# Kernel tuning notes

Measured on AMD Instinct MI355X. Metric: run time of the kernel, lower is better.

The kernel has to match this reference:

```python
import jax, jax.numpy as jnp
import numpy as np

D_MODEL = 1024
NUM_HEADS = 16
D_K = D_MODEL // NUM_HEADS
THETA = 10000.0


def _apply_rope(x, positions):
    # x: [B, H, S, d_k], positions: [B, S]
    dk = x.shape[-1]
    freq = 1.0 / (THETA ** (jnp.arange(0, dk, 2, dtype=jnp.float32) / dk))  # [dk/2]
    ang = positions.astype(jnp.float32)[:, None, :, None] * freq  # [B,1,S,dk/2]
    cos, sin = jnp.cos(ang), jnp.sin(ang)
    x_even = x[..., 0::2]
    x_odd = x[..., 1::2]
    re = x_even * cos - x_odd * sin
    ro = x_even * sin + x_odd * cos
    # interleave back: [..., dk/2, 2] -> [..., dk]
    return jnp.stack([re, ro], axis=-1).reshape(x.shape)


def setup_inputs() -> dict:
    key = jax.random.key(0)
    kx, kq, kk, kv, ko = jax.random.split(key, 5)
    B, S = 2, 2048
    std = (2.0 / (D_MODEL + D_MODEL)) ** 0.5
    x = jax.random.normal(kx, (B, S, D_MODEL), dtype=jnp.float32)
    Wq = jax.random.normal(kq, (D_MODEL, D_MODEL), dtype=jnp.float32) * std
    Wk = jax.random.normal(kk, (D_MODEL, D_MODEL), dtype=jnp.float32) * std
    Wv = jax.random.normal(kv, (D_MODEL, D_MODEL), dtype=jnp.float32) * std
    Wo = jax.random.normal(ko, (D_MODEL, D_MODEL), dtype=jnp.float32) * std
    token_positions = jnp.tile(jnp.arange(S, dtype=jnp.int32)[None, :], (B, 1))
    return {"x": x, "Wq": Wq, "Wk": Wk, "Wv": Wv, "Wo": Wo,
            "token_positions": token_positions}


def reference(x, Wq, Wk, Wv, Wo, token_positions):
    B, S, D = x.shape
    H, dk = NUM_HEADS, D_K
    scale = 1.0 / np.sqrt(dk)
    # Linear is y = x @ W.T with W:[d_out, d_in]
    q = jnp.einsum('bsd,ed->bse', x, Wq).reshape(B, S, H, dk).transpose(0, 2, 1, 3)
    k = jnp.einsum('bsd,ed->bse', x, Wk).reshape(B, S, H, dk).transpose(0, 2, 1, 3)
    v = jnp.einsum('bsd,ed->bse', x, Wv).reshape(B, S, H, dk).transpose(0, 2, 1, 3)
    q = _apply_rope(q, token_positions)
    k = _apply_rope(k, token_positions)
    scores = jnp.einsum('bhqd,bhkd->bhqk', q, k) * scale  # [B,H,S,S]
    causal = jnp.tril(jnp.ones((S, S), dtype=bool))
    scores = jnp.where(causal[None, None, :, :], scores, -jnp.inf)
    probs = jax.nn.softmax(scores, axis=-1)
    attn = jnp.einsum('bhqk,bhkd->bhqd', probs, v)  # [B,H,S,dk]
    attn = attn.transpose(0, 2, 1, 3).reshape(B, S, D)
    return jnp.einsum('bsd,ed->bse', attn, Wo)
```

## Files before the change

### kernel.cpp

```cpp
#include <hip/hip_runtime.h>
#include <hip/hip_bf16.h>
#include <math.h>

#define B_  2
#define S_  2048
#define H_  16
#define D_  1024
#define DK_ 64

typedef __attribute__((ext_vector_type(8))) short bf16x8;
typedef __attribute__((ext_vector_type(8))) unsigned short ushort8v;
typedef __attribute__((ext_vector_type(4))) float f32x4;

__device__ __forceinline__ unsigned short f2bf(float f) {
  unsigned u = __float_as_uint(f);
  unsigned r = (u + 0x7FFFu + ((u >> 16) & 1u)) >> 16;
  return (unsigned short)r;
}
__device__ __forceinline__ unsigned pack_trunc(float lo, float hi) {
  return (__float_as_uint(lo) >> 16) | (__float_as_uint(hi) & 0xffff0000u);
}
__device__ __forceinline__ float fast_exp2(float x) {
#if __has_builtin(__builtin_amdgcn_exp2f)
  return __builtin_amdgcn_exp2f(x);
#else
  return __expf(x * 0.69314718056f);
#endif
}
__device__ __forceinline__ void gload_lds16(const unsigned short* g,
                                            unsigned short* l) {
  __builtin_amdgcn_global_load_lds(
      (const __attribute__((address_space(1))) unsigned int*)(const void*)g,
      (__attribute__((address_space(3))) unsigned int*)(void*)l, 16, 0, 0);
}

__global__ __launch_bounds__(256)
void cast5_bf16(const float* __restrict__ x,  const float* __restrict__ wq,
                const float* __restrict__ wk, const float* __restrict__ wv,
                const float* __restrict__ wo,
                unsigned short* __restrict__ xb,  unsigned short* __restrict__ wqb,
                unsigned short* __restrict__ wkb, unsigned short* __restrict__ wvb,
                unsigned short* __restrict__ wob)
{
  const int idx = blockIdx.x;
  const float* s; unsigned short* d; int lblk;
  if (idx < 2048) { s = x; d = xb; lblk = idx; }
  else {
    int t = idx - 2048;
    int w = t >> 9;
    lblk  = t & 511;
    s = (w == 0) ? wq  : (w == 1) ? wk  : (w == 2) ? wv  : wo;
    d = (w == 0) ? wqb : (w == 1) ? wkb : (w == 2) ? wvb : wob;
  }
  size_t i0 = ((size_t)lblk * 256 + threadIdx.x) * 8;
  float4 v0 = *(const float4*)(s + i0);
  float4 v1 = *(const float4*)(s + i0 + 4);
  ushort8v o;
  o[0] = f2bf(v0.x); o[1] = f2bf(v0.y); o[2] = f2bf(v0.z); o[3] = f2bf(v0.w);
  o[4] = f2bf(v1.x); o[5] = f2bf(v1.y); o[6] = f2bf(v1.z); o[7] = f2bf(v1.w);
  *(ushort8v*)(d + i0) = o;
}

__global__ __launch_bounds__(256)
void gemm_qkv(const unsigned short* __restrict__ A0,
              const unsigned short* __restrict__ W0,
              const unsigned short* __restrict__ W1,
              const unsigned short* __restrict__ W2,
              unsigned short* __restrict__ qh,
              unsigned short* __restrict__ kh,
              unsigned short* __restrict__ vt,
              const int* __restrict__ tp)
{
  const int z    = blockIdx.z;
  const int flat = blockIdx.y * 8 + blockIdx.x;
  const int xcd  = flat & 7;
  const int u    = flat >> 3;

  int row0, col0;
  if (z < 2) {
    row0 = (xcd * 8 + (u & 7)) * 64;
    col0 = (u >> 3) * 128;
  } else {
    int tc = xcd * 4 + (u & 3);
    int cr = u >> 2;
    row0 = cr * 64;
    col0 = tc * 128;
  }
  const unsigned short* Aptr = (z == 2) ? W2 : A0;
  const unsigned short* Bptr = (z == 0) ? W0 : (z == 1) ? W1 : A0;

  __shared__ unsigned short As[64 * 64];
  __shared__ unsigned short Bs[128 * 64];
  __shared__ int tps[64];

  const int tid   = threadIdx.x;
  const int wave  = tid >> 6;
  const int lane  = tid & 63;
  const int quad  = lane >> 4;
  const int col16 = lane & 15;
  const int wr    = (wave >> 1) * 32;
  const int wc    = (wave & 1) * 64;

  if (z < 2 && tid < 64) tps[tid] = tp[row0 + tid];

  const int srow = wave * 8 + (lane >> 3);
  const int scol = ((lane & 7) ^ ((lane >> 3) & 7)) * 8;
  const unsigned short* gA = Aptr + (size_t)(row0 + srow) * D_ + scol;
  const unsigned short* gB = Bptr + (size_t)(col0 + srow) * D_ + scol;

  f32x4 acc[2][4];
  #pragma unroll
  for (int mt = 0; mt < 2; ++mt)
    #pragma unroll
    for (int nt = 0; nt < 4; ++nt)
      #pragma unroll
      for (int r = 0; r < 4; ++r) acc[mt][nt][r] = 0.f;

  for (int k0 = 0; k0 < D_; k0 += 64) {
    __syncthreads();
    #pragma unroll
    for (int p = 0; p < 2; ++p)
      gload_lds16(gA + (size_t)(p * 32) * D_ + k0, &As[(p * 32 + wave * 8) * 64]);
    #pragma unroll
    for (int p = 0; p < 4; ++p)
      gload_lds16(gB + (size_t)(p * 32) * D_ + k0, &Bs[(p * 32 + wave * 8) * 64]);
    __syncthreads();

    #pragma unroll
    for (int h = 0; h < 2; ++h) {
      const int jo = ((h * 4 + quad) ^ (col16 & 7)) * 8;
      bf16x8 af[2], bfr[4];
      #pragma unroll
      for (int mt = 0; mt < 2; ++mt)
        af[mt] = *(const bf16x8*)&As[(wr + mt * 16 + col16) * 64 + jo];
      #pragma unroll
      for (int nt = 0; nt < 4; ++nt)
        bfr[nt] = *(const bf16x8*)&Bs[(wc + nt * 16 + col16) * 64 + jo];

      #pragma unroll
      for (int mt = 0; mt < 2; ++mt)
        #pragma unroll
        for (int nt = 0; nt < 4; ++nt)
          acc[mt][nt] = __builtin_amdgcn_mfma_f32_16x16x32_bf16(
              af[mt], bfr[nt], acc[mt][nt], 0, 0, 0);
    }
  }

  if (z == 2) {
    #pragma unroll
    for (int mt = 0; mt < 2; ++mt)
      #pragma unroll
      for (int r = 0; r < 4; ++r) {
        int c = row0 + wr + mt * 16 + quad * 4 + r;
        int h = c >> 6, d = c & 63;
        #pragma unroll
        for (int nt = 0; nt < 4; ++nt) {
          int t  = col0 + wc + nt * 16 + col16;
          int bb = t >> 11, sl = t & (S_ - 1);
          vt[((size_t)((bb << 4) + h) * DK_ + d) * S_ + sl] =
              f2bf(acc[mt][nt][r]);
        }
      }
  } else {
    unsigned short* C = z ? kh : qh;
    const float qs = z ? 1.0f : 0.1803368801111204f;
    const float sgn = (col16 & 1) ? 1.f : -1.f;
    float freqr[4];
    #pragma unroll
    for (int nt = 0; nt < 4; ++nt) {
      int i = ((wc + nt * 16 + col16) & 63) >> 1;
      freqr[nt] = exp2f(-0.4152410118f * (float)i);
    }
    #pragma unroll
    for (int mt = 0; mt < 2; ++mt)
      #pragma unroll
      for (int r = 0; r < 4; ++r) {
        int rl  = wr + mt * 16 + quad * 4 + r;
        int row = row0 + rl;
        float p = (float)tps[rl];
        #pragma unroll
        for (int nt = 0; nt < 4; ++nt) {
          int col = col0 + wc + nt * 16 + col16;
          float ang = p * freqr[nt];
          float sn = __sinf(ang), cs = __cosf(ang);
          float val = acc[mt][nt][r];
          float oth = __shfl_xor(val, 1);
          C[(size_t)row * D_ + col] = f2bf((val * cs + oth * sgn * sn) * qs);
        }
      }
  }
}

__global__ __launch_bounds__(256, 8)
void gemm_wo(const unsigned short* __restrict__ A,
             const unsigned short* __restrict__ W,
             float* __restrict__ C)
{
  __shared__ unsigned short As[64 * 64];
  __shared__ unsigned short Bs[64 * 64];

  const int flat = blockIdx.y * 16 + blockIdx.x;
  const int xcd  = flat & 7;
  const int u    = flat >> 3;
  const int by   = xcd * 8 + (u & 7);
  const int bx   = u >> 3;

  const int tid   = threadIdx.x;
  const int wave  = tid >> 6;
  const int lane  = tid & 63;
  const int quad  = lane >> 4;
  const int col16 = lane & 15;
  const int row0  = by * 64;
  const int col0  = bx * 64;
  const int wr    = (wave >> 1) * 32;
  const int wc    = (wave & 1) * 32;

  const int srow = wave * 8 + (lane >> 3);
  const int scol = ((lane & 7) ^ ((lane >> 3) & 7)) * 8;
  const unsigned short* gA = A + (size_t)(row0 + srow) * D_ + scol;
  const unsigned short* gB = W + (size_t)(col0 + srow) * D_ + scol;

  f32x4 acc[2][2];
  #pragma unroll
  for (int mt = 0; mt < 2; ++mt)
    #pragma unroll
    for (int nt = 0; nt < 2; ++nt)
      #pragma unroll
      for (int r = 0; r < 4; ++r) acc[mt][nt][r] = 0.f;

  for (int k0 = 0; k0 < D_; k0 += 64) {
    __syncthreads();
    #pragma unroll
    for (int p = 0; p < 2; ++p) {
      gload_lds16(gA + (size_t)(p * 32) * D_ + k0, &As[(p * 32 + wave * 8) * 64]);
      gload_lds16(gB + (size_t)(p * 32) * D_ + k0, &Bs[(p * 32 + wave * 8) * 64]);
    }
    __syncthreads();

    #pragma unroll
    for (int h = 0; h < 2; ++h) {
      const int jo = ((h * 4 + quad) ^ (col16 & 7)) * 8;
      bf16x8 af[2], bfr[2];
      #pragma unroll
      for (int mt = 0; mt < 2; ++mt)
        af[mt] = *(const bf16x8*)&As[(wr + mt * 16 + col16) * 64 + jo];
      #pragma unroll
      for (int nt = 0; nt < 2; ++nt)
        bfr[nt] = *(const bf16x8*)&Bs[(wc + nt * 16 + col16) * 64 + jo];

      #pragma unroll
      for (int mt = 0; mt < 2; ++mt)
        #pragma unroll
        for (int nt = 0; nt < 2; ++nt)
          acc[mt][nt] = __builtin_amdgcn_mfma_f32_16x16x32_bf16(
              af[mt], bfr[nt], acc[mt][nt], 0, 0, 0);
    }
  }

  #pragma unroll
  for (int mt = 0; mt < 2; ++mt)
    #pragma unroll
    for (int r = 0; r < 4; ++r) {
      int row = row0 + wr + mt * 16 + quad * 4 + r;
      #pragma unroll
      for (int nt = 0; nt < 2; ++nt) {
        int col = col0 + wc + nt * 16 + col16;
        C[(size_t)row * D_ + col] = acc[mt][nt][r];
      }
    }
}

__global__ __launch_bounds__(512, 8)
void attn_mfma(const unsigned short* __restrict__ Q,
               const unsigned short* __restrict__ K,
               const unsigned short* __restrict__ Vt,
               unsigned short* __restrict__ O)
{
  const int f   = blockIdx.x;
  const int qt  = 31 - (f >> 5);
  const int bh  = f & 31;
  const int b   = bh >> 4, h = bh & 15;

  const int tid  = threadIdx.x;
  const int w    = tid >> 6;
  const int lane = tid & 63;
  const int quad = lane >> 4;
  const int col  = lane & 15;
  const int rw   = w & 3;
  const int p    = w >> 2;
  const int qlocal = rw * 16 + col;

  __shared__ unsigned short Ks[2 * 4096];
  __shared__ unsigned short Vs[2 * 4096];
  __shared__ __align__(16) unsigned short Pl[8][16][72];

  const size_t qkbase = (size_t)b * S_ * D_ + (size_t)h * DK_;
  const size_t vtbase = (size_t)bh * DK_ * S_;

  const int qrow = qt * 64 + qlocal;
  bf16x8 qf[2];
  qf[0] = *(const bf16x8*)(Q + qkbase + (size_t)qrow * D_ + quad * 8);
  qf[1] = *(const bf16x8*)(Q + qkbase + (size_t)qrow * D_ + 32 + quad * 8);

  const int lr8 = lane >> 3;
  const int sj  = ((lane & 7) ^ (lr8 & 7)) * 8;

  auto stageK = [&](int g) {
    const int gc = (g > qt) ? qt : g;
    const unsigned short* s =
        K + qkbase + (size_t)(gc * 64 + rw * 16 + lr8) * D_ + sj;
    #pragma unroll
    for (int pp = 0; pp < 2; ++pp)
      gload_lds16(s + (size_t)(pp * 8) * D_, &Ks[p * 4096 + (rw * 16 + pp * 8) * 64]);
  };
  auto stageV = [&](int g) {
    const int gc = (g > qt) ? qt : g;
    const unsigned short* s =
        Vt + vtbase + (size_t)(rw * 16 + lr8) * S_ + gc * 64 + sj;
    #pragma unroll
    for (int pp = 0; pp < 2; ++pp)
      gload_lds16(s + (size_t)(pp * 8) * S_, &Vs[p * 4096 + (rw * 16 + pp * 8) * 64]);
  };

  f32x4 Oacc[4];
  #pragma unroll
  for (int nb = 0; nb < 4; ++nb)
    #pragma unroll
    for (int r = 0; r < 4; ++r) Oacc[nb][r] = 0.f;
  float l_i = 0.f;

  const int M  = (qt >> 1) + 1;
  const int jx = quad ^ (col & 7);
  const unsigned short* KsH = Ks + p * 4096;
  const unsigned short* VsH = Vs + p * 4096;
  unsigned short (*Plw)[72] = Pl[w];

  stageK(p);
  stageV(p);
  asm volatile("s_waitcnt vmcnt(0)" ::: "memory");
  __builtin_amdgcn_s_barrier();
  __builtin_amdgcn_sched_barrier(0);

  for (int m = 0; m < M; ++m) {
    const int g    = 2 * m + p;
    const bool act = (g <= qt);
    const bool dg  = (g == qt);

    f32x4 st[4];
    if (act) {
      __builtin_amdgcn_s_setprio(1);
      #pragma unroll
      for (int nb = 0; nb < 4; ++nb) {
        const int s0 = (nb * 16 + col) * 8 + jx;
        bf16x8 ka0 = *(const bf16x8*)(KsH + s0 * 8);
        bf16x8 ka1 = *(const bf16x8*)(KsH + (s0 ^ 4) * 8);
        f32x4 a = {-24.f, -24.f, -24.f, -24.f};
        a = __builtin_amdgcn_mfma_f32_16x16x32_bf16(ka0, qf[0], a, 0, 0, 0);
        a = __builtin_amdgcn_mfma_f32_16x16x32_bf16(ka1, qf[1], a, 0, 0, 0);
        st[nb] = a;
      }
      __builtin_amdgcn_s_setprio(0);
    }
    __builtin_amdgcn_sched_barrier(0);
    __builtin_amdgcn_s_barrier();
    __builtin_amdgcn_sched_barrier(0);

    stageK(2 * m + 2 + p);

    if (act) {
      if (dg) {
        #pragma unroll
        for (int nb = 0; nb < 4; ++nb)
          #pragma unroll
          for (int r = 0; r < 4; ++r)
            if (nb * 16 + quad * 4 + r > qlocal) st[nb][r] = -1e30f;
      }
      float rsum = 0.f;
      #pragma unroll
      for (int nb = 0; nb < 4; ++nb)
        #pragma unroll
        for (int r = 0; r < 4; ++r) {
          float pv = fast_exp2(st[nb][r]);
          st[nb][r] = pv;
          rsum += pv;
        }
      rsum += __shfl_xor(rsum, 16);
      rsum += __shfl_xor(rsum, 32);
      l_i += rsum;
      #pragma unroll
      for (int nb = 0; nb < 4; ++nb) {
        uint2 pk;
        pk.x = pack_trunc(st[nb][0], st[nb][1]);
        pk.y = pack_trunc(st[nb][2], st[nb][3]);
        *(uint2*)&Plw[col][nb * 16 + quad * 4] = pk;
      }
    }

    asm volatile("s_waitcnt vmcnt(2)" ::: "memory");
    __builtin_amdgcn_sched_barrier(0);
    __builtin_amdgcn_s_barrier();
    __builtin_amdgcn_sched_barrier(0);

    if (act) {
      bf16x8 pf0 = *(const bf16x8*)&Plw[col][quad * 8];
      bf16x8 pf1 = *(const bf16x8*)&Plw[col][32 + quad * 8];
      __builtin_amdgcn_s_setprio(1);
      #pragma unroll
      for (int nb = 0; nb < 4; ++nb) {
        const int s0 = (nb * 16 + col) * 8 + jx;
        bf16x8 va0 = *(const bf16x8*)(VsH + s0 * 8);
        bf16x8 va1 = *(const bf16x8*)(VsH + (s0 ^ 4) * 8);
        Oacc[nb] = __builtin_amdgcn_mfma_f32_16x16x32_bf16(va0, pf0, Oacc[nb], 0, 0, 0);
        Oacc[nb] = __builtin_amdgcn_mfma_f32_16x16x32_bf16(va1, pf1, Oacc[nb], 0, 0, 0);
      }
      __builtin_amdgcn_s_setprio(0);
    }
    __builtin_amdgcn_sched_barrier(0);
    __builtin_amdgcn_s_barrier();
    __builtin_amdgcn_sched_barrier(0);

    stageV(2 * m + 2 + p);
    asm volatile("s_waitcnt vmcnt(2)" ::: "memory");
    __builtin_amdgcn_sched_barrier(0);
    __builtin_amdgcn_s_barrier();
    __builtin_amdgcn_sched_barrier(0);
  }

  asm volatile("s_waitcnt vmcnt(0)" ::: "memory");
  __syncthreads();
  float* sc = (float*)&Pl[0][0][0];
  if (p == 1) {
    float* d0 = sc + ((size_t)(rw * 64 + lane)) * 18;
    #pragma unroll
    for (int nb = 0; nb < 4; ++nb)
      #pragma unroll
      for (int r = 0; r < 4; ++r) d0[nb * 4 + r] = Oacc[nb][r];
    d0[16] = l_i;
  }
  __syncthreads();
  if (p == 0) {
    const float* s0 = sc + ((size_t)(rw * 64 + lane)) * 18;
    const float inv = 1.0f / (l_i + s0[16]);
    #pragma unroll
    for (int nb = 0; nb < 4; ++nb) {
      int d = nb * 16 + quad * 4;
      ushort4 oa;
      oa.x = f2bf((Oacc[nb][0] + s0[nb * 4 + 0]) * inv);
      oa.y = f2bf((Oacc[nb][1] + s0[nb * 4 + 1]) * inv);
      oa.z = f2bf((Oacc[nb][2] + s0[nb * 4 + 2]) * inv);
      oa.w = f2bf((Oacc[nb][3] + s0[nb * 4 + 3]) * inv);
      *(ushort4*)(O + (size_t)b * S_ * D_ + (size_t)qrow * D_ + h * DK_ + d) = oa;
    }
  }
}

extern "C" void kernel_launch(void* const* d_in, const int* in_sizes, int n_in,
                              void* d_out, int out_size, void* d_ws, size_t ws_size,
                              hipStream_t stream)
{
  const float* x  = (const float*)d_in[0];
  const float* Wq = (const float*)d_in[1];
  const float* Wk = (const float*)d_in[2];
  const float* Wv = (const float*)d_in[3];
  const float* Wo = (const float*)d_in[4];
  const int*   tp = (const int*)d_in[5];
  float* out = (float*)d_out;

  const size_t NTOK = (size_t)B_ * S_ * D_;
  const size_t NW   = (size_t)D_ * D_;
  unsigned short* qh  = (unsigned short*)d_ws;
  unsigned short* kh  = qh + NTOK;
  unsigned short* vt  = kh + NTOK;
  unsigned short* xb  = vt + NTOK;
  unsigned short* wqb = xb + NTOK;
  unsigned short* wkb = wqb + NW;
  unsigned short* wvb = wkb + NW;
  unsigned short* wob = wvb + NW;
  unsigned short* ab  = xb;

  cast5_bf16<<<dim3(4096), 256, 0, stream>>>(
      x, Wq, Wk, Wv, Wo, xb, wqb, wkb, wvb, wob);

  gemm_qkv<<<dim3(8, 64, 3), 256, 0, stream>>>(
      xb, wqb, wkb, wvb, qh, kh, vt, tp);

  attn_mfma<<<dim3(32 * 32), 512, 0, stream>>>(qh, kh, vt, ab);

  gemm_wo<<<dim3(16, 64), 256, 0, stream>>>(ab, wob, out);
}
```

Measured before the change: 169.4 us.

## Drop LDS staging of K/V in attention; load fragments directly from global

Removes the double-buffered LDS staging of K and V tiles and the per-iteration block barriers. Each wave now loads its K and V MFMA fragments straight from global memory, relying on L1/L2 for reuse across the four waves that share a tile. It also drops the occupancy hint in launch_bounds. The intent is to remove barrier and LDS overhead, at the cost of redundant global/L2 traffic and more exposed load latency with no software prefetch.

```diff
diff --git a/kernel.cpp b/kernel.cpp
--- a/kernel.cpp
+++ b/kernel.cpp
@@ -270,7 +270,7 @@
     }
 }
 
-__global__ __launch_bounds__(512, 8)
+__global__ __launch_bounds__(512)
 void attn_mfma(const unsigned short* __restrict__ Q,
                const unsigned short* __restrict__ K,
                const unsigned short* __restrict__ Vt,
@@ -290,8 +290,6 @@
   const int p    = w >> 2;
   const int qlocal = rw * 16 + col;
 
-  __shared__ unsigned short Ks[2 * 4096];
-  __shared__ unsigned short Vs[2 * 4096];
   __shared__ __align__(16) unsigned short Pl[8][16][72];
 
   const size_t qkbase = (size_t)b * S_ * D_ + (size_t)h * DK_;
@@ -302,26 +300,6 @@
   qf[0] = *(const bf16x8*)(Q + qkbase + (size_t)qrow * D_ + quad * 8);
   qf[1] = *(const bf16x8*)(Q + qkbase + (size_t)qrow * D_ + 32 + quad * 8);
 
-  const int lr8 = lane >> 3;
-  const int sj  = ((lane & 7) ^ (lr8 & 7)) * 8;
-
-  auto stageK = [&](int g) {
-    const int gc = (g > qt) ? qt : g;
-    const unsigned short* s =
-        K + qkbase + (size_t)(gc * 64 + rw * 16 + lr8) * D_ + sj;
-    #pragma unroll
-    for (int pp = 0; pp < 2; ++pp)
-      gload_lds16(s + (size_t)(pp * 8) * D_, &Ks[p * 4096 + (rw * 16 + pp * 8) * 64]);
-  };
-  auto stageV = [&](int g) {
-    const int gc = (g > qt) ? qt : g;
-    const unsigned short* s =
-        Vt + vtbase + (size_t)(rw * 16 + lr8) * S_ + gc * 64 + sj;
-    #pragma unroll
-    for (int pp = 0; pp < 2; ++pp)
-      gload_lds16(s + (size_t)(pp * 8) * S_, &Vs[p * 4096 + (rw * 16 + pp * 8) * 64]);
-  };
-
   f32x4 Oacc[4];
   #pragma unroll
   for (int nb = 0; nb < 4; ++nb)
@@ -329,104 +307,66 @@
     for (int r = 0; r < 4; ++r) Oacc[nb][r] = 0.f;
   float l_i = 0.f;
 
-  const int M  = (qt >> 1) + 1;
-  const int jx = quad ^ (col & 7);
-  const unsigned short* KsH = Ks + p * 4096;
-  const unsigned short* VsH = Vs + p * 4096;
+  const unsigned short* Kg = K + qkbase;
+  const unsigned short* Vg = Vt + vtbase;
   unsigned short (*Plw)[72] = Pl[w];
 
-  stageK(p);
-  stageV(p);
-  asm volatile("s_waitcnt vmcnt(0)" ::: "memory");
-  __builtin_amdgcn_s_barrier();
-  __builtin_amdgcn_sched_barrier(0);
-
-  for (int m = 0; m < M; ++m) {
-    const int g    = 2 * m + p;
-    const bool act = (g <= qt);
-    const bool dg  = (g == qt);
+  for (int g = p; g <= qt; g += 2) {
+    const bool dg = (g == qt);
 
     f32x4 st[4];
-    if (act) {
-      __builtin_amdgcn_s_setprio(1);
-      #pragma unroll
-      for (int nb = 0; nb < 4; ++nb) {
-        const int s0 = (nb * 16 + col) * 8 + jx;
-        bf16x8 ka0 = *(const bf16x8*)(KsH + s0 * 8);
-        bf16x8 ka1 = *(const bf16x8*)(KsH + (s0 ^ 4) * 8);
-        f32x4 a = {-24.f, -24.f, -24.f, -24.f};
-        a = __builtin_amdgcn_mfma_f32_16x16x32_bf16(ka0, qf[0], a, 0, 0, 0);
-        a = __builtin_amdgcn_mfma_f32_16x16x32_bf16(ka1, qf[1], a, 0, 0, 0);
-        st[nb] = a;
-      }
-      __builtin_amdgcn_s_setprio(0);
-    }
-    __builtin_amdgcn_sched_barrier(0);
-    __builtin_amdgcn_s_barrier();
-    __builtin_amdgcn_sched_barrier(0);
-
-    stageK(2 * m + 2 + p);
-
-    if (act) {
-      if (dg) {
-        #pragma unroll
-        for (int nb = 0; nb < 4; ++nb)
-          #pragma unroll
-          for (int r = 0; r < 4; ++r)
-            if (nb * 16 + quad * 4 + r > qlocal) st[nb][r] = -1e30f;
-      }
-      float rsum = 0.f;
+    #pragma unroll
+    for (int nb = 0; nb < 4; ++nb) {
+      const unsigned short* kr =
+          Kg + (size_t)(g * 64 + nb * 16 + col) * D_ + quad * 8;
+      bf16x8 ka0 = *(const bf16x8*)kr;
+      bf16x8 ka1 = *(const bf16x8*)(kr + 32);
+      f32x4 a = {-24.f, -24.f, -24.f, -24.f};
+      a = __builtin_amdgcn_mfma_f32_16x16x32_bf16(ka0, qf[0], a, 0, 0, 0);
+      a = __builtin_amdgcn_mfma_f32_16x16x32_bf16(ka1, qf[1], a, 0, 0, 0);
+      st[nb] = a;
+    }
+
+    if (dg) {
       #pragma unroll
       for (int nb = 0; nb < 4; ++nb)
         #pragma unroll
-        for (int r = 0; r < 4; ++r) {
-          float pv = fast_exp2(st[nb][r]);
-          st[nb][r] = pv;
-          rsum += pv;
-        }
-      rsum += __shfl_xor(rsum, 16);
-      rsum += __shfl_xor(rsum, 32);
-      l_i += rsum;
-      #pragma unroll
-      for (int nb = 0; nb < 4; ++nb) {
-        uint2 pk;
-        pk.x = pack_trunc(st[nb][0], st[nb][1]);
-        pk.y = pack_trunc(st[nb][2], st[nb][3]);
-        *(uint2*)&Plw[col][nb * 16 + quad * 4] = pk;
+        for (int r = 0; r < 4; ++r)
+          if (nb * 16 + quad * 4 + r > qlocal) st[nb][r] = -1e30f;
+    }
+    float rsum = 0.f;
+    #pragma unroll
+    for (int nb = 0; nb < 4; ++nb)
+      #pragma unroll
+      for (int r = 0; r < 4; ++r) {
+        float pv = fast_exp2(st[nb][r]);
+        st[nb][r] = pv;
+        rsum += pv;
       }
-    }
-
-    asm volatile("s_waitcnt vmcnt(2)" ::: "memory");
-    __builtin_amdgcn_sched_barrier(0);
-    __builtin_amdgcn_s_barrier();
-    __builtin_amdgcn_sched_barrier(0);
-
-    if (act) {
-      bf16x8 pf0 = *(const bf16x8*)&Plw[col][quad * 8];
-      bf16x8 pf1 = *(const bf16x8*)&Plw[col][32 + quad * 8];
-      __builtin_amdgcn_s_setprio(1);
-      #pragma unroll
-      for (int nb = 0; nb < 4; ++nb) {
-        const int s0 = (nb * 16 + col) * 8 + jx;
-        bf16x8 va0 = *(const bf16x8*)(VsH + s0 * 8);
-        bf16x8 va1 = *(const bf16x8*)(VsH + (s0 ^ 4) * 8);
-        Oacc[nb] = __builtin_amdgcn_mfma_f32_16x16x32_bf16(va0, pf0, Oacc[nb], 0, 0, 0);
-        Oacc[nb] = __builtin_amdgcn_mfma_f32_16x16x32_bf16(va1, pf1, Oacc[nb], 0, 0, 0);
-      }
-      __builtin_amdgcn_s_setprio(0);
-    }
-    __builtin_amdgcn_sched_barrier(0);
-    __builtin_amdgcn_s_barrier();
-    __builtin_amdgcn_sched_barrier(0);
-
-    stageV(2 * m + 2 + p);
-    asm volatile("s_waitcnt vmcnt(2)" ::: "memory");
-    __builtin_amdgcn_sched_barrier(0);
-    __builtin_amdgcn_s_barrier();
-    __builtin_amdgcn_sched_barrier(0);
-  }
-
-  asm volatile("s_waitcnt vmcnt(0)" ::: "memory");
+    rsum += __shfl_xor(rsum, 16);
+    rsum += __shfl_xor(rsum, 32);
+    l_i += rsum;
+    #pragma unroll
+    for (int nb = 0; nb < 4; ++nb) {
+      uint2 pk;
+      pk.x = pack_trunc(st[nb][0], st[nb][1]);
+      pk.y = pack_trunc(st[nb][2], st[nb][3]);
+      *(uint2*)&Plw[col][nb * 16 + quad * 4] = pk;
+    }
+    bf16x8 pf0 = *(const bf16x8*)&Plw[col][quad * 8];
+    bf16x8 pf1 = *(const bf16x8*)&Plw[col][32 + quad * 8];
+
+    #pragma unroll
+    for (int nb = 0; nb < 4; ++nb) {
+      const unsigned short* vr =
+          Vg + (size_t)(nb * 16 + col) * S_ + g * 64 + quad * 8;
+      bf16x8 va0 = *(const bf16x8*)vr;
+      bf16x8 va1 = *(const bf16x8*)(vr + 32);
+      Oacc[nb] = __builtin_amdgcn_mfma_f32_16x16x32_bf16(va0, pf0, Oacc[nb], 0, 0, 0);
+      Oacc[nb] = __builtin_amdgcn_mfma_f32_16x16x32_bf16(va1, pf1, Oacc[nb], 0, 0, 0);
+    }
+  }
+
   __syncthreads();
   float* sc = (float*)&Pl[0][0][0];
   if (p == 1) {
```

Measured after the change: 262.4 us. 1.55x slower.

## Fuse Q and K projections into one block sharing the X tile

Applied to the files above, without the earlier changes.

The Q and K GEMMs are merged so that each block loads the activation tile once and multiplies it against both Wq and Wk tiles, keeping two accumulator sets and applying RoPE to both in the epilogue. The grid shrinks from three z-slices to two, and the V slice keeps its own path. This cuts the redundant activation loads and LDS traffic per MFMA, at the cost of more LDS per block (a second B buffer) and twice the accumulator registers in the fused path. It also adds a launch-bounds occupancy hint and leaves an uneven workload between the z-slices.

```diff
diff --git a/kernel.cpp b/kernel.cpp
--- a/kernel.cpp
+++ b/kernel.cpp
@@ -61,7 +61,7 @@
   *(ushort8v*)(d + i0) = o;
 }
 
-__global__ __launch_bounds__(256)
+__global__ __launch_bounds__(256, 4)
 void gemm_qkv(const unsigned short* __restrict__ A0,
               const unsigned short* __restrict__ W0,
               const unsigned short* __restrict__ W1,
@@ -76,21 +76,9 @@
   const int xcd  = flat & 7;
   const int u    = flat >> 3;
 
-  int row0, col0;
-  if (z < 2) {
-    row0 = (xcd * 8 + (u & 7)) * 64;
-    col0 = (u >> 3) * 128;
-  } else {
-    int tc = xcd * 4 + (u & 3);
-    int cr = u >> 2;
-    row0 = cr * 64;
-    col0 = tc * 128;
-  }
-  const unsigned short* Aptr = (z == 2) ? W2 : A0;
-  const unsigned short* Bptr = (z == 0) ? W0 : (z == 1) ? W1 : A0;
-
   __shared__ unsigned short As[64 * 64];
-  __shared__ unsigned short Bs[128 * 64];
+  __shared__ unsigned short Bs0[128 * 64];
+  __shared__ unsigned short Bs1[128 * 64];
   __shared__ int tps[64];
 
   const int tid   = threadIdx.x;
@@ -101,52 +89,137 @@
   const int wr    = (wave >> 1) * 32;
   const int wc    = (wave & 1) * 64;
 
-  if (z < 2 && tid < 64) tps[tid] = tp[row0 + tid];
-
   const int srow = wave * 8 + (lane >> 3);
   const int scol = ((lane & 7) ^ ((lane >> 3) & 7)) * 8;
-  const unsigned short* gA = Aptr + (size_t)(row0 + srow) * D_ + scol;
-  const unsigned short* gB = Bptr + (size_t)(col0 + srow) * D_ + scol;
-
-  f32x4 acc[2][4];
-  #pragma unroll
-  for (int mt = 0; mt < 2; ++mt)
-    #pragma unroll
-    for (int nt = 0; nt < 4; ++nt)
-      #pragma unroll
-      for (int r = 0; r < 4; ++r) acc[mt][nt][r] = 0.f;
-
-  for (int k0 = 0; k0 < D_; k0 += 64) {
-    __syncthreads();
-    #pragma unroll
-    for (int p = 0; p < 2; ++p)
-      gload_lds16(gA + (size_t)(p * 32) * D_ + k0, &As[(p * 32 + wave * 8) * 64]);
-    #pragma unroll
-    for (int p = 0; p < 4; ++p)
-      gload_lds16(gB + (size_t)(p * 32) * D_ + k0, &Bs[(p * 32 + wave * 8) * 64]);
-    __syncthreads();
-
-    #pragma unroll
-    for (int h = 0; h < 2; ++h) {
-      const int jo = ((h * 4 + quad) ^ (col16 & 7)) * 8;
-      bf16x8 af[2], bfr[4];
-      #pragma unroll
-      for (int mt = 0; mt < 2; ++mt)
-        af[mt] = *(const bf16x8*)&As[(wr + mt * 16 + col16) * 64 + jo];
+
+  if (z == 0) {
+    const int row0 = (xcd * 8 + (u & 7)) * 64;
+    const int col0 = (u >> 3) * 128;
+
+    if (tid < 64) tps[tid] = tp[row0 + tid];
+
+    const unsigned short* gA  = A0 + (size_t)(row0 + srow) * D_ + scol;
+    const unsigned short* gB0 = W0 + (size_t)(col0 + srow) * D_ + scol;
+    const unsigned short* gB1 = W1 + (size_t)(col0 + srow) * D_ + scol;
+
+    f32x4 accq[2][4], acck[2][4];
+    #pragma unroll
+    for (int mt = 0; mt < 2; ++mt)
       #pragma unroll
       for (int nt = 0; nt < 4; ++nt)
-        bfr[nt] = *(const bf16x8*)&Bs[(wc + nt * 16 + col16) * 64 + jo];
-
-      #pragma unroll
-      for (int mt = 0; mt < 2; ++mt)
+        #pragma unroll
+        for (int r = 0; r < 4; ++r) { accq[mt][nt][r] = 0.f; acck[mt][nt][r] = 0.f; }
+
+    for (int k0 = 0; k0 < D_; k0 += 64) {
+      __syncthreads();
+      #pragma unroll
+      for (int p = 0; p < 2; ++p)
+        gload_lds16(gA + (size_t)(p * 32) * D_ + k0, &As[(p * 32 + wave * 8) * 64]);
+      #pragma unroll
+      for (int p = 0; p < 4; ++p) {
+        gload_lds16(gB0 + (size_t)(p * 32) * D_ + k0, &Bs0[(p * 32 + wave * 8) * 64]);
+        gload_lds16(gB1 + (size_t)(p * 32) * D_ + k0, &Bs1[(p * 32 + wave * 8) * 64]);
+      }
+      __syncthreads();
+
+      #pragma unroll
+      for (int h = 0; h < 2; ++h) {
+        const int jo = ((h * 4 + quad) ^ (col16 & 7)) * 8;
+        bf16x8 af[2];
+        #pragma unroll
+        for (int mt = 0; mt < 2; ++mt)
+          af[mt] = *(const bf16x8*)&As[(wr + mt * 16 + col16) * 64 + jo];
+        #pragma unroll
+        for (int nt = 0; nt < 4; ++nt) {
+          bf16x8 bq = *(const bf16x8*)&Bs0[(wc + nt * 16 + col16) * 64 + jo];
+          #pragma unroll
+          for (int mt = 0; mt < 2; ++mt)
+            accq[mt][nt] = __builtin_amdgcn_mfma_f32_16x16x32_bf16(
+                af[mt], bq, accq[mt][nt], 0, 0, 0);
+          bf16x8 bk = *(const bf16x8*)&Bs1[(wc + nt * 16 + col16) * 64 + jo];
+          #pragma unroll
+          for (int mt = 0; mt < 2; ++mt)
+            acck[mt][nt] = __builtin_amdgcn_mfma_f32_16x16x32_bf16(
+                af[mt], bk, acck[mt][nt], 0, 0, 0);
+        }
+      }
+    }
+
+    const float qs  = 0.1803368801111204f;
+    const float sgn = (col16 & 1) ? 1.f : -1.f;
+    float freqr[4];
+    #pragma unroll
+    for (int nt = 0; nt < 4; ++nt) {
+      int i = ((wc + nt * 16 + col16) & 63) >> 1;
+      freqr[nt] = exp2f(-0.4152410118f * (float)i);
+    }
+    #pragma unroll
+    for (int mt = 0; mt < 2; ++mt)
+      #pragma unroll
+      for (int r = 0; r < 4; ++r) {
+        int rl  = wr + mt * 16 + quad * 4 + r;
+        int row = row0 + rl;
+        float p = (float)tps[rl];
+        #pragma unroll
+        for (int nt = 0; nt < 4; ++nt) {
+          int col = col0 + wc + nt * 16 + col16;
+          float ang = p * freqr[nt];
+          float sn = __sinf(ang), cs = __cosf(ang);
+          float vq = accq[mt][nt][r];
+          float oq = __shfl_xor(vq, 1);
+          qh[(size_t)row * D_ + col] = f2bf((vq * cs + oq * sgn * sn) * qs);
+          float vk = acck[mt][nt][r];
+          float ok = __shfl_xor(vk, 1);
+          kh[(size_t)row * D_ + col] = f2bf(vk * cs + ok * sgn * sn);
+        }
+      }
+  } else {
+    const int tc   = xcd * 4 + (u & 3);
+    const int cr   = u >> 2;
+    const int row0 = cr * 64;
+    const int col0 = tc * 128;
+
+    const unsigned short* gA = W2 + (size_t)(row0 + srow) * D_ + scol;
+    const unsigned short* gB = A0 + (size_t)(col0 + srow) * D_ + scol;
+
+    f32x4 acc[2][4];
+    #pragma unroll
+    for (int mt = 0; mt < 2; ++mt)
+      #pragma unroll
+      for (int nt = 0; nt < 4; ++nt)
+        #pragma unroll
+        for (int r = 0; r < 4; ++r) acc[mt][nt][r] = 0.f;
+
+    for (int k0 = 0; k0 < D_; k0 += 64) {
+      __syncthreads();
+      #pragma unroll
+      for (int p = 0; p < 2; ++p)
+        gload_lds16(gA + (size_t)(p * 32) * D_ + k0, &As[(p * 32 + wave * 8) * 64]);
+      #pragma unroll
+      for (int p = 0; p < 4; ++p)
+        gload_lds16(gB + (size_t)(p * 32) * D_ + k0, &Bs0[(p * 32 + wave * 8) * 64]);
+      __syncthreads();
+
+      #pragma unroll
+      for (int h = 0; h < 2; ++h) {
+        const int jo = ((h * 4 + quad) ^ (col16 & 7)) * 8;
+        bf16x8 af[2], bfr[4];
+        #pragma unroll
+        for (int mt = 0; mt < 2; ++mt)
+          af[mt] = *(const bf16x8*)&As[(wr + mt * 16 + col16) * 64 + jo];
         #pragma unroll
         for (int nt = 0; nt < 4; ++nt)
-          acc[mt][nt] = __builtin_amdgcn_mfma_f32_16x16x32_bf16(
-              af[mt], bfr[nt], acc[mt][nt], 0, 0, 0);
-    }
-  }
-
-  if (z == 2) {
+          bfr[nt] = *(const bf16x8*)&Bs0[(wc + nt * 16 + col16) * 64 + jo];
+
+        #pragma unroll
+        for (int mt = 0; mt < 2; ++mt)
+          #pragma unroll
+          for (int nt = 0; nt < 4; ++nt)
+            acc[mt][nt] = __builtin_amdgcn_mfma_f32_16x16x32_bf16(
+                af[mt], bfr[nt], acc[mt][nt], 0, 0, 0);
+      }
+    }
+
     #pragma unroll
     for (int mt = 0; mt < 2; ++mt)
       #pragma unroll
@@ -159,33 +232,6 @@
           int bb = t >> 11, sl = t & (S_ - 1);
           vt[((size_t)((bb << 4) + h) * DK_ + d) * S_ + sl] =
               f2bf(acc[mt][nt][r]);
-        }
-      }
-  } else {
-    unsigned short* C = z ? kh : qh;
-    const float qs = z ? 1.0f : 0.1803368801111204f;
-    const float sgn = (col16 & 1) ? 1.f : -1.f;
-    float freqr[4];
-    #pragma unroll
-    for (int nt = 0; nt < 4; ++nt) {
-      int i = ((wc + nt * 16 + col16) & 63) >> 1;
-      freqr[nt] = exp2f(-0.4152410118f * (float)i);
-    }
-    #pragma unroll
-    for (int mt = 0; mt < 2; ++mt)
-      #pragma unroll
-      for (int r = 0; r < 4; ++r) {
-        int rl  = wr + mt * 16 + quad * 4 + r;
-        int row = row0 + rl;
-        float p = (float)tps[rl];
-        #pragma unroll
-        for (int nt = 0; nt < 4; ++nt) {
-          int col = col0 + wc + nt * 16 + col16;
-          float ang = p * freqr[nt];
-          float sn = __sinf(ang), cs = __cosf(ang);
-          float val = acc[mt][nt][r];
-          float oth = __shfl_xor(val, 1);
-          C[(size_t)row * D_ + col] = f2bf((val * cs + oth * sgn * sn) * qs);
         }
       }
   }
@@ -481,7 +527,7 @@
   cast5_bf16<<<dim3(4096), 256, 0, stream>>>(
       x, Wq, Wk, Wv, Wo, xb, wqb, wkb, wvb, wob);
 
-  gemm_qkv<<<dim3(8, 64, 3), 256, 0, stream>>>(
+  gemm_qkv<<<dim3(8, 64, 2), 256, 0, stream>>>(
       xb, wqb, wkb, wvb, qh, kh, vt, tp);
 
   attn_mfma<<<dim3(32 * 32), 512, 0, stream>>>(qh, kh, vt, ab);
```

Measured after the change: 172.9 us. 2.1% more time.
